# Kernel optimization log

Hardware: AMD Instinct MI355X
Metric: run time of the kernel (lower is better)

Reference implementation:

```python
import jax, jax.numpy as jnp
import numpy as np

D_MODEL = 1024
N_HEADS = 16
D_HEAD = D_MODEL // N_HEADS
D_FF = 4096
BATCH = 2
SEQ = 2048
EPS = 1e-5


def setup_inputs() -> dict:
    key = jax.random.key(0)
    ks = jax.random.split(key, 8)
    s = 0.02
    x = jax.random.normal(ks[0], (BATCH, SEQ, D_MODEL), dtype=jnp.float32)
    # Per-head projection weights, stacked: [H, d_head, d_model] (torch Linear stores (out,in))
    wq = jax.random.normal(ks[1], (N_HEADS, D_HEAD, D_MODEL), dtype=jnp.float32) * s
    wk = jax.random.normal(ks[2], (N_HEADS, D_HEAD, D_MODEL), dtype=jnp.float32) * s
    wv = jax.random.normal(ks[3], (N_HEADS, D_HEAD, D_MODEL), dtype=jnp.float32) * s
    wo = jax.random.normal(ks[4], (D_MODEL, D_MODEL), dtype=jnp.float32) * s
    w1 = jax.random.normal(ks[5], (D_FF, D_MODEL), dtype=jnp.float32) * s
    w2 = jax.random.normal(ks[6], (D_MODEL, D_FF), dtype=jnp.float32) * s
    ln1_g = jnp.ones((D_MODEL,), jnp.float32)
    ln1_b = jnp.zeros((D_MODEL,), jnp.float32)
    ln2_g = jnp.ones((D_MODEL,), jnp.float32)
    ln2_b = jnp.zeros((D_MODEL,), jnp.float32)
    return {"x": x, "wq": wq, "wk": wk, "wv": wv, "wo": wo,
            "w1": w1, "w2": w2, "ln1_g": ln1_g, "ln1_b": ln1_b,
            "ln2_g": ln2_g, "ln2_b": ln2_b}


def _layer_norm(x, g, b):
    mu = jnp.mean(x, axis=-1, keepdims=True)
    var = jnp.mean(jnp.square(x - mu), axis=-1, keepdims=True)
    return (x - mu) * jax.lax.rsqrt(var + EPS) * g + b


def _mha(h, wq, wk, wv, wo):
    # h: [b,s,d]; wq/wk/wv: [H,dh,d] -> q/k/v: [b,H,s,dh]
    q = jnp.einsum('bsd,hed->bhse', h, wq)
    k = jnp.einsum('bsd,hed->bhse', h, wk)
    v = jnp.einsum('bsd,hed->bhse', h, wv)
    scores = jnp.einsum('bhqe,bhke->bhqk', q, k) / jnp.sqrt(jnp.float32(D_HEAD))
    weights = jax.nn.softmax(scores, axis=-1)
    ctx = jnp.einsum('bhqk,bhke->bhqe', weights, v)  # [b,H,s,dh]
    # concat heads in order (head 0 first) -> [b,s,H*dh]
    concat = jnp.transpose(ctx, (0, 2, 1, 3)).reshape(h.shape[0], h.shape[1], D_MODEL)
    return concat @ wo.T


def reference(x, wq, wk, wv, wo, w1, w2, ln1_g, ln1_b, ln2_g, ln2_b):
    h = _layer_norm(x, ln1_g, ln1_b)
    attn_out = _mha(h, wq, wk, wv, wo)
    h2 = _layer_norm(x + attn_out, ln2_g, ln2_b)
    ff = jax.nn.gelu(h2 @ w1.T, approximate=False) @ w2.T
    return x + ff
```

## Files before the change

kernel.cpp:

```cpp
#include <hip/hip_runtime.h>
#include <hip/hip_bf16.h>
#include <math.h>

typedef __bf16 bf16_t;
typedef __bf16 bf16x8 __attribute__((ext_vector_type(8)));
typedef __bf16 bf16x4 __attribute__((ext_vector_type(4)));
typedef float f32x4 __attribute__((ext_vector_type(4)));
typedef unsigned int u32;
typedef u32 u32x2 __attribute__((ext_vector_type(2)));

#define DM 1024
#define SEQL 2048
#define NTOK 4096
#define QKVN 3072

__device__ __forceinline__ void gload_lds16(const bf16_t* g, bf16_t* l){
  __builtin_amdgcn_global_load_lds((const __attribute__((address_space(1))) void*)g,
                                   (__attribute__((address_space(3))) void*)l, 16, 0, 0);
}
__device__ __forceinline__ u32 ldsoff(const void* p){
  return (u32)(size_t)(__attribute__((address_space(3))) const void*)p;
}
__device__ __forceinline__ u32x2 tr64(u32 byte_off){
  u32x2 d;
  asm volatile("ds_read_b64_tr_b16 %0, %1" : "=v"(d) : "v"(byte_off));
  return d;
}
__device__ __forceinline__ u32 pack2(float a, float b){
  union{ __bf16 h[2]; u32 w; } z;
  z.h[0]=(__bf16)a; z.h[1]=(__bf16)b; return z.w;
}
__device__ __forceinline__ float gelu_fast(float x){
  const float y = 0.79788456f*(x + 0.044715f*x*x*x);
  float a = y*2.885390082f;
  a = fminf(fmaxf(a, -30.f), 30.f);
  const float t = __builtin_amdgcn_exp2f(a);
  const float th = (t-1.0f)*__builtin_amdgcn_rcpf(t+1.0f);
  return 0.5f*x*(1.0f+th);
}

__global__ __launch_bounds__(256) void prep_kernel(
    const float* __restrict__ wq, const float* __restrict__ wk,
    const float* __restrict__ wv, const float* __restrict__ wo,
    const float* __restrict__ w1, const float* __restrict__ w2,
    const float* __restrict__ x,  const float* __restrict__ g1,
    const float* __restrict__ b1,
    bf16_t* __restrict__ wqkv_b, bf16_t* __restrict__ wo_b,
    bf16_t* __restrict__ w1_b,   bf16_t* __restrict__ w2_b,
    bf16_t* __restrict__ h1)
{
  __shared__ float red[8];
  const int bid = blockIdx.x;
  const int t = threadIdx.x;
  if (bid < 12288){
    const int flat = (bid*256 + t)*4;
    const int seg = flat >> 20;
    const int off1m = flat & 1048575;
    const float* src; bf16_t* dst;
    if (seg < 3){
      src = (seg==0 ? wq : (seg==1 ? wk : wv)) + off1m;
      dst = wqkv_b + flat;
    } else if (seg == 3){
      src = wo + off1m;  dst = wo_b + off1m;
    } else if (seg < 8){
      src = w1 + (flat - 4*1048576);  dst = w1_b + (flat - 4*1048576);
    } else {
      src = w2 + (flat - 8*1048576);  dst = w2_b + (flat - 8*1048576);
    }
    const float4 v = *(const float4*)src;
    bf16x4 o; o[0]=(__bf16)v.x; o[1]=(__bf16)v.y; o[2]=(__bf16)v.z; o[3]=(__bf16)v.w;
    *(bf16x4*)dst = o;
  } else {
    const int row = bid - 12288;
    const float4 v = *(const float4*)(x + (size_t)row*DM + t*4);
    float s  = v.x+v.y+v.z+v.w;
    float sq = v.x*v.x+v.y*v.y+v.z*v.z+v.w*v.w;
    #pragma unroll
    for (int m=1;m<64;m<<=1){ s += __shfl_xor(s,m); sq += __shfl_xor(sq,m); }
    const int w = t>>6;
    if ((t&63)==0){ red[w]=s; red[4+w]=sq; }
    __syncthreads();
    s  = red[0]+red[1]+red[2]+red[3];
    sq = red[4]+red[5]+red[6]+red[7];
    const float mean = s*(1.f/DM);
    const float var  = sq*(1.f/DM) - mean*mean;
    const float rstd = rsqrtf(var + 1e-5f);
    const float4 gg = *(const float4*)(g1 + t*4);
    const float4 bb = *(const float4*)(b1 + t*4);
    bf16x4 o;
    o[0]=(__bf16)((v.x-mean)*rstd*gg.x+bb.x);
    o[1]=(__bf16)((v.y-mean)*rstd*gg.y+bb.y);
    o[2]=(__bf16)((v.z-mean)*rstd*gg.z+bb.z);
    o[3]=(__bf16)((v.w-mean)*rstd*gg.w+bb.w);
    *(bf16x4*)(h1 + (size_t)row*DM + t*4) = o;
  }
}

__global__ __launch_bounds__(256) void lnb_kernel(const bf16_t* __restrict__ in,
    const float* __restrict__ g, const float* __restrict__ bta,
    bf16_t* __restrict__ outp)
{
  const int row = blockIdx.x;
  const int t = threadIdx.x;
  const bf16x4 raw = *(const bf16x4*)(in + (size_t)row*DM + t*4);
  float4 v;
  v.x=(float)raw[0]; v.y=(float)raw[1]; v.z=(float)raw[2]; v.w=(float)raw[3];
  float s  = v.x+v.y+v.z+v.w;
  float sq = v.x*v.x+v.y*v.y+v.z*v.z+v.w*v.w;
  #pragma unroll
  for (int m=1;m<64;m<<=1){ s += __shfl_xor(s,m); sq += __shfl_xor(sq,m); }
  __shared__ float red[8];
  const int w = t>>6;
  if ((t&63)==0){ red[w]=s; red[4+w]=sq; }
  __syncthreads();
  s  = red[0]+red[1]+red[2]+red[3];
  sq = red[4]+red[5]+red[6]+red[7];
  const float mean = s*(1.f/DM);
  const float var  = sq*(1.f/DM) - mean*mean;
  const float rstd = rsqrtf(var + 1e-5f);
  const float4 gg = *(const float4*)(g + t*4);
  const float4 bb = *(const float4*)(bta + t*4);
  bf16x4 o;
  o[0]=(__bf16)((v.x-mean)*rstd*gg.x+bb.x);
  o[1]=(__bf16)((v.y-mean)*rstd*gg.y+bb.y);
  o[2]=(__bf16)((v.z-mean)*rstd*gg.z+bb.z);
  o[3]=(__bf16)((v.w-mean)*rstd*gg.w+bb.w);
  *(bf16x4*)(outp + (size_t)row*DM + t*4) = o;
}

__global__ __launch_bounds__(256) void red4_kernel(
    const bf16_t* __restrict__ p0, const bf16_t* __restrict__ p1,
    const bf16_t* __restrict__ p2, const bf16_t* __restrict__ p3,
    const float* __restrict__ x, float* __restrict__ outp)
{
  const int i = (blockIdx.x*256 + threadIdx.x)*8;
  const bf16x8 a0 = *(const bf16x8*)(p0 + i);
  const bf16x8 a1 = *(const bf16x8*)(p1 + i);
  const bf16x8 a2 = *(const bf16x8*)(p2 + i);
  const bf16x8 a3 = *(const bf16x8*)(p3 + i);
  #pragma unroll
  for (int h=0; h<2; h++){
    const float4 xs = *(const float4*)(x + i + h*4);
    float4 o;
    o.x = xs.x + ((float)a0[h*4+0]+(float)a1[h*4+0]) + ((float)a2[h*4+0]+(float)a3[h*4+0]);
    o.y = xs.y + ((float)a0[h*4+1]+(float)a1[h*4+1]) + ((float)a2[h*4+1]+(float)a3[h*4+1]);
    o.z = xs.z + ((float)a0[h*4+2]+(float)a1[h*4+2]) + ((float)a2[h*4+2]+(float)a3[h*4+2]);
    o.w = xs.w + ((float)a0[h*4+3]+(float)a1[h*4+3]) + ((float)a2[h*4+3]+(float)a3[h*4+3]);
    *(float4*)(outp + i + h*4) = o;
  }
}

template<int EPI>
__global__ __launch_bounds__(512, 2) void gemm8ph(
    const bf16_t* __restrict__ A, const bf16_t* __restrict__ Bw,
    void* __restrict__ c0, void* __restrict__ c1,
    void* __restrict__ c2, void* __restrict__ c3,
    int N, int K, int lda)
{
  __shared__ __align__(16) char ldsb[131072];
  const int tid = threadIdx.x, lane = tid&63, wid = tid>>6;
  const int q16 = lane&15, g = lane>>4;
  const int wm = wid>>2, wn = wid&3;

  const int flat = blockIdx.y*gridDim.x + blockIdx.x;
  const int xcd = flat&7, jj = flat>>3;
  const int NY = gridDim.y;
  const int jdiv = jj/NY, jmod = jj - jdiv*NY;
  const int bm = (xcd*2 + jdiv)*256, bn = jmod*256;
  const int sk = blockIdx.z;
  const int koff = sk*K;
  void* Cout = (sk==0) ? c0 : (sk==1) ? c1 : (sk==2) ? c2 : c3;

  int mloc, kloc;
  {
    const u32 L = tid*16;
    const u32 logical = L ^ (((L>>9)&1)<<5);
    mloc = (int)(logical>>6);
    kloc = (int)((logical&63)>>1);
  }
  const bf16_t* asrc = A  + (size_t)(bm + mloc)*lda + koff + kloc;
  const bf16_t* bsrc = Bw + (size_t)(bn + mloc)*lda + koff + kloc;
  const u32 laneOff = ((u32)(q16*64 + g*16)) ^ ((u32)(q16&8)<<2);

  f32x4 acc[8][4] = {};
  bf16x8 bv[4];

  auto stage = [&](int buf, int kh, int isB, int s){
    const bf16_t* src = isB ? bsrc : asrc;
    #pragma unroll
    for (int h2=0; h2<2; h2++)
      gload_lds16(src + (size_t)(h2*128)*lda + s*64 + kh*32,
                  (bf16_t*)(ldsb + buf*65536 + isB*32768 + kh*16384 + h2*8192 + tid*16));
  };

  stage(0,0,0,0); stage(0,0,1,0); stage(0,1,0,0); stage(0,1,1,0);
  stage(1,0,0,1); stage(1,0,1,1);
  asm volatile("s_waitcnt vmcnt(4)" ::: "memory");
  __builtin_amdgcn_s_barrier();

  const int NSTEP = K>>6;
  const int NIT = NSTEP>>1;

#define PHASE(BUF,KH,MH,DOST,SBUF,SKH,SISB,SSTEP,CK) { \
    bf16x8 av[4]; \
    const char* Ab_ = ldsb + (BUF)*65536 + (KH)*16384 + wm*8192; \
    _Pragma("unroll") for (int jx=0;jx<4;jx++) \
      av[jx] = *(const bf16x8*)(Ab_ + (((MH)*4+jx)<<10) + laneOff); \
    if ((MH)==0){ \
      const char* Bb_ = ldsb + (BUF)*65536 + 32768 + (KH)*16384 + (wn>>1)*8192; \
      _Pragma("unroll") for (int jx=0;jx<4;jx++) \
        bv[jx] = *(const bf16x8*)(Bb_ + ((((wn&1)*4)+jx)<<10) + laneOff); \
    } \
    if (DOST) stage(SBUF,SKH,SISB,SSTEP); \
    asm volatile("s_barrier" ::: "memory"); \
    asm volatile("s_waitcnt lgkmcnt(0)" ::: "memory"); \
    __builtin_amdgcn_s_setprio(1); \
    _Pragma("unroll") for (int jx=0;jx<4;jx++) \
      _Pragma("unroll") for (int j2=0;j2<4;j2++) \
        acc[(MH)*4+jx][j2] = __builtin_amdgcn_mfma_f32_16x16x32_bf16(av[jx], bv[j2], acc[(MH)*4+jx][j2],0,0,0); \
    __builtin_amdgcn_s_setprio(0); \
    if (CK){ if (nl) { asm volatile("s_waitcnt vmcnt(4)" ::: "memory"); } \
             else    { asm volatile("s_waitcnt vmcnt(0)" ::: "memory"); } } \
    asm volatile("s_barrier" ::: "memory"); }

  for (int it=0; it<NIT; it++){
    const int s0 = 2*it, s1 = s0+1;
    const bool nl = (it+1 < NIT);
    PHASE(0,0,0, 1,  1,1,0, s1,   0)
    PHASE(0,0,1, 1,  1,1,1, s1,   0)
    PHASE(0,1,0, nl, 0,0,0, s0+2, 0)
    PHASE(0,1,1, nl, 0,0,1, s0+2, 1)
    PHASE(1,0,0, nl, 0,1,0, s0+2, 0)
    PHASE(1,0,1, nl, 0,1,1, s0+2, 0)
    PHASE(1,1,0, nl, 1,0,0, s1+2, 0)
    PHASE(1,1,1, nl, 1,0,1, s1+2, 1)
  }
#undef PHASE

  #pragma unroll
  for (int fm=0; fm<8; fm++)
    #pragma unroll
    for (int fn=0; fn<4; fn++)
      #pragma unroll
      for (int i=0; i<4; i++){
        const int r = bm + wm*128 + fm*16 + g*4 + i;
        const int c = bn + wn*64 + fn*16 + q16;
        const size_t idx = (size_t)r*N + c;
        const float vv = acc[fm][fn][i];
        if constexpr (EPI==0){
          ((bf16_t*)Cout)[idx] = (__bf16)vv;
        } else {
          ((bf16_t*)Cout)[idx] = (__bf16)gelu_fast(vv);
        }
      }
}

template<int EPI>
__global__ __launch_bounds__(512, 2) void gemm128(
    const bf16_t* __restrict__ A, const bf16_t* __restrict__ Bw,
    void* __restrict__ Cout, const float* __restrict__ X,
    int N, int K)
{
  constexpr int BK = 32;
  __shared__ __align__(16) char ldsb[3*16384];
  const int tid = threadIdx.x, lane = tid&63, wid = tid>>6;
  const int q16 = lane&15, g = lane>>4;
  const int wm = wid>>2, wn = wid&3;

  const int flat = blockIdx.y*gridDim.x + blockIdx.x;
  const int xcd = flat&7, j = flat>>3;
  const int bm = ((xcd<<2) + (j>>3))*128, bn = (j&7)*128;

  int mloc, kloc;
  {
    const u32 L = tid*16;
    const u32 logical = L ^ (((L>>9)&1)<<5);
    mloc = (int)(logical>>6);
    kloc = (int)((logical&63)>>1);
  }
  const bf16_t* asrc = A  + (size_t)(bm + mloc)*K + kloc;
  const bf16_t* bsrc = Bw + (size_t)(bn + mloc)*K + kloc;
  const u32 laneOff = ((u32)(q16*64 + g*16)) ^ ((u32)(q16&8)<<2);

  f32x4 acc[4][2] = {};

  auto stageA = [&](int buf, int k0){
    gload_lds16(asrc + k0, (bf16_t*)(ldsb + buf*16384 + tid*16));
  };
  auto stageB = [&](int buf, int k0){
    gload_lds16(bsrc + k0, (bf16_t*)(ldsb + buf*16384 + 8192 + tid*16));
  };

  stageA(0,0); stageB(0,0);
  stageA(1,BK); stageB(1,BK);
  asm volatile("s_waitcnt vmcnt(2)" ::: "memory");
  __builtin_amdgcn_s_barrier();

  const int NT = K/BK;
  int bcur = 0;
  for (int kt=0; kt<NT; kt++){
    const int bstg = (bcur >= 1) ? bcur-1 : bcur+2;
    const char* Ab = ldsb + bcur*16384 + wm*4096;
    const char* Bb = ldsb + bcur*16384 + 8192 + wn*2048;
    const bool sOK = (kt+2 < NT);
    const int k0s = (kt+2)*BK;
    bf16x8 bv[2];
    #pragma unroll
    for (int p=0; p<2; p++){
      bf16x8 av[2];
      #pragma unroll
      for (int jx=0;jx<2;jx++)
        av[jx] = *(const bf16x8*)(Ab + ((p*2+jx)<<10) + laneOff);
      if (p==0){
        #pragma unroll
        for (int jx=0;jx<2;jx++)
          bv[jx] = *(const bf16x8*)(Bb + (jx<<10) + laneOff);
      }
      if (sOK){
        if (p==0) stageA(bstg,k0s);
        else      stageB(bstg,k0s);
      }
      asm volatile("s_barrier" ::: "memory");
      __builtin_amdgcn_s_setprio(1);
      #pragma unroll
      for (int jx=0;jx<2;jx++)
        #pragma unroll
        for (int j2=0;j2<2;j2++)
          acc[p*2+jx][j2] = __builtin_amdgcn_mfma_f32_16x16x32_bf16(av[jx], bv[j2], acc[p*2+jx][j2], 0,0,0);
      __builtin_amdgcn_s_setprio(0);
      if (p==1){
        if (sOK) asm volatile("s_waitcnt vmcnt(2)" ::: "memory");
        else     asm volatile("s_waitcnt vmcnt(0)" ::: "memory");
      }
      asm volatile("s_barrier" ::: "memory");
    }
    bcur = (bcur==2)?0:bcur+1;
  }

  #pragma unroll
  for (int fm=0; fm<4; fm++)
    #pragma unroll
    for (int fn=0; fn<2; fn++)
      #pragma unroll
      for (int i=0; i<4; i++){
        const int r = bm + wm*64 + fm*16 + g*4 + i;
        const int c = bn + wn*32 + fn*16 + q16;
        const size_t idx = (size_t)r*N + c;
        const float vv = X[idx] + acc[fm][fn][i];
        ((bf16_t*)Cout)[idx] = (__bf16)vv;
      }
}

__global__ __launch_bounds__(512, 4) void attn_kernel(
    const bf16_t* __restrict__ QKV, bf16_t* __restrict__ Ctx)
{
  __shared__ __align__(16) bf16_t Ks[2][128*64];
  __shared__ __align__(16) bf16_t Vs[2][32*4*72];
  const int tid = threadIdx.x, lane = tid&63, w = tid>>6;
  const int g = lane>>4, q16 = lane&15;
  const int bh = blockIdx.y, b = bh>>4, h = bh&15;
  const int qr0 = blockIdx.x*128 + w*16;
  const size_t tok0 = (size_t)b*SEQL;
  const int ch0 = h*64;

  bf16x8 aq[2];
  #pragma unroll
  for (int ks=0; ks<2; ks++){
    bf16x8 t = *(const bf16x8*)(QKV + (tok0+qr0+q16)*QKVN + ch0 + ks*32 + g*8);
    #pragma unroll
    for (int jx=0;jx<8;jx++) t[jx] = (__bf16)((float)t[jx]*0.18033688f);
    aq[ks] = t;
  }

  const int srow = tid>>3, sc8 = (tid&7)*8;
  const bf16_t* kptr_swz = QKV + (tok0+srow)*QKVN + 1024 + ch0 + (sc8 ^ ((srow&7)<<3));
  const bf16_t* vptr = QKV + (tok0+srow)*QKVN + 2048 + ch0 + sc8;
  const int vwoff = ((srow>>2)*4 + (sc8>>4))*72 + (srow&3)*16 + (sc8&15);

  float mrun = -1e30f, lrun = 0.f;
  f32x4 o[4] = {};

  #pragma unroll
  for (int it=0; it<2; it++)
    gload_lds16(kptr_swz + (size_t)(it*64)*QKVN, &Ks[0][tid*8 + it*4096]);
  bf16x8 vreg[2];
  #pragma unroll
  for (int it=0; it<2; it++)
    vreg[it] = *(const bf16x8*)(vptr + (size_t)(it*64)*QKVN);
  #pragma unroll
  for (int it=0; it<2; it++)
    *(bf16x8*)&Vs[0][vwoff + it*4608] = vreg[it];
  #pragma unroll
  for (int it=0; it<2; it++)
    vreg[it] = *(const bf16x8*)(vptr + (size_t)(128 + it*64)*QKVN);

  const int NT = SEQL/128;
  for (int t=0; t<NT; t++){
    __syncthreads();
    if (t+1 < NT){
      #pragma unroll
      for (int it=0; it<2; it++){
        gload_lds16(kptr_swz + (size_t)((t+1)*128 + it*64)*QKVN, &Ks[(t+1)&1][tid*8 + it*4096]);
        *(bf16x8*)&Vs[(t+1)&1][vwoff + it*4608] = vreg[it];
      }
      if (t+2 < NT){
        #pragma unroll
        for (int it=0; it<2; it++)
          vreg[it] = *(const bf16x8*)(vptr + (size_t)((t+2)*128 + it*64)*QKVN);
      }
    }
    const bf16_t* ksb = Ks[t&1];
    const u32 vs0 = ldsoff(&Vs[t&1][0]);

    f32x4 s[8] = {};
    __builtin_amdgcn_s_setprio(1);
    #pragma unroll
    for (int ks=0; ks<2; ks++){
      #pragma unroll
      for (int fn=0; fn<8; fn++){
        const int r = fn*16 + q16;
        const int ce = ks*32 + g*8;
        bf16x8 bk = *(const bf16x8*)&ksb[r*64 + (ce ^ ((r&7)<<3))];
        s[fn] = __builtin_amdgcn_mfma_f32_16x16x32_bf16(bk, aq[ks], s[fn], 0, 0, 0);
      }
    }
    __builtin_amdgcn_s_setprio(0);

    float mx = -1e30f;
    #pragma unroll
    for (int fn=0; fn<8; fn++){
      const float a = fmaxf(fmaxf(s[fn][0], s[fn][1]), s[fn][2]);
      mx = fmaxf(fmaxf(mx, a), s[fn][3]);
    }
    mx = fmaxf(mx, __shfl_xor(mx,16));
    mx = fmaxf(mx, __shfl_xor(mx,32));

    if (!__all(mx <= mrun + 11.54f)){
      const float mnew = fmaxf(mrun, mx);
      const float alpha = __builtin_amdgcn_exp2f(mrun - mnew);
      #pragma unroll
      for (int i=0;i<4;i++){
        const float ai = __shfl(alpha, g*4+i);
        o[0][i]*=ai; o[1][i]*=ai; o[2][i]*=ai; o[3][i]*=ai;
      }
      lrun *= alpha;
      mrun = mnew;
    }

    float rs = 0.f;
    u32 u[8][2];
    #pragma unroll
    for (int fn=0; fn<8; fn++){
      const float e0=__builtin_amdgcn_exp2f(s[fn][0]-mrun);
      const float e1=__builtin_amdgcn_exp2f(s[fn][1]-mrun);
      const float e2=__builtin_amdgcn_exp2f(s[fn][2]-mrun);
      const float e3=__builtin_amdgcn_exp2f(s[fn][3]-mrun);
      rs += (e0+e1)+(e2+e3);
      u[fn][0] = pack2(e0,e1);
      u[fn][1] = pack2(e2,e3);
    }
    rs += __shfl_xor(rs,16);
    rs += __shfl_xor(rs,32);
    lrun += rs;

    {
      u32x2 loA[4], hiA[4], loB[4], hiB[4];
      #pragma unroll
      for (int ne=0; ne<4; ne++){
        const u32 vb = vs0 + (u32)(((2*g*4 + ne)*72 + q16)*2);
        loA[ne] = tr64(vb);
        hiA[ne] = tr64(vb + 576);
      }
      #pragma unroll
      for (int ks=0; ks<4; ks++){
        union { u32 wd[4]; bf16x8 v; } pa;
        #pragma unroll
        for (int jj=0; jj<4; jj++){
          const int src = q16 + ((((g&1)<<1) + (jj>>1))<<4);
          const u32 a0 = (u32)__shfl((int)u[2*ks  ][jj&1], src);
          const u32 a1 = (u32)__shfl((int)u[2*ks+1][jj&1], src);
          pa.wd[jj] = (g&2) ? a1 : a0;
        }
        if (ks < 3){
          u32x2* nl_ = (ks&1) ? loA : loB;
          u32x2* nh_ = (ks&1) ? hiA : hiB;
          #pragma unroll
          for (int ne=0; ne<4; ne++){
            const u32 vb = vs0 + (u32)(((((ks+1)*8 + 2*g)*4 + ne)*72 + q16)*2);
            nl_[ne] = tr64(vb);
            nh_[ne] = tr64(vb + 576);
          }
          asm volatile("s_waitcnt lgkmcnt(8)" ::: "memory");
        } else {
          asm volatile("s_waitcnt lgkmcnt(0)" ::: "memory");
        }
        __builtin_amdgcn_sched_barrier(0);
        const u32x2* lo = (ks&1) ? loB : loA;
        const u32x2* hi = (ks&1) ? hiB : hiA;
        union { u32x2 u2[2]; bf16x8 v; } cc;
        __builtin_amdgcn_s_setprio(1);
        #pragma unroll
        for (int ne=0; ne<4; ne++){
          cc.u2[0]=lo[ne]; cc.u2[1]=hi[ne];
          o[ne] = __builtin_amdgcn_mfma_f32_16x16x32_bf16(pa.v, cc.v, o[ne], 0, 0, 0);
        }
        __builtin_amdgcn_s_setprio(0);
      }
    }
  }

  const float rl = 1.0f/lrun;
  #pragma unroll
  for (int i=0; i<4; i++){
    const float ri = __shfl(rl, g*4+i);
    #pragma unroll
    for (int ne=0; ne<4; ne++){
      const int r = qr0 + g*4 + i;
      Ctx[(tok0+r)*DM + ch0 + ne*16 + q16] = (__bf16)(o[ne][i]*ri);
    }
  }
}

extern "C" void kernel_launch(void* const* d_in, const int* in_sizes, int n_in,
                              void* d_out, int out_size, void* d_ws, size_t ws_size,
                              hipStream_t stream)
{
  (void)in_sizes; (void)n_in; (void)out_size; (void)ws_size;
  const float* x  = (const float*)d_in[0];
  const float* wq = (const float*)d_in[1];
  const float* wk = (const float*)d_in[2];
  const float* wv = (const float*)d_in[3];
  const float* wo = (const float*)d_in[4];
  const float* w1 = (const float*)d_in[5];
  const float* w2 = (const float*)d_in[6];
  const float* g1 = (const float*)d_in[7];
  const float* b1 = (const float*)d_in[8];
  const float* g2 = (const float*)d_in[9];
  const float* b2 = (const float*)d_in[10];
  float* out = (float*)d_out;
  char* ws = (char*)d_ws;
  const size_t MB = 1024ull*1024ull;

  bf16_t* wqkv_b = (bf16_t*)(ws);
  bf16_t* wo_b   = (bf16_t*)(ws + 6*MB);
  bf16_t* w1_b   = (bf16_t*)(ws + 8*MB);
  bf16_t* w2_b   = (bf16_t*)(ws + 16*MB);
  bf16_t* h1     = (bf16_t*)(ws + 24*MB);
  bf16_t* qkv    = (bf16_t*)(ws + 32*MB);
  bf16_t* ctx    = (bf16_t*)(ws + 56*MB);
  bf16_t* res2b  = (bf16_t*)(ws + 64*MB);
  bf16_t* h2     = h1;
  bf16_t* ffm    = (bf16_t*)(ws + 32*MB);
  bf16_t* p0     = (bf16_t*)(ws);
  bf16_t* p1     = (bf16_t*)(ws + 8*MB);
  bf16_t* p2     = (bf16_t*)(ws + 24*MB);
  bf16_t* p3     = (bf16_t*)(ws + 64*MB);

  prep_kernel<<<16384, 256, 0, stream>>>(wq, wk, wv, wo, w1, w2, x, g1, b1,
                                         wqkv_b, wo_b, w1_b, w2_b, h1);
  gemm8ph<0><<<dim3(16, 12), 512, 0, stream>>>(h1, wqkv_b, (void*)qkv, (void*)qkv,
                                               (void*)qkv, (void*)qkv, QKVN, 1024, 1024);
  attn_kernel<<<dim3(16, 32), 512, 0, stream>>>(qkv, ctx);
  gemm128<0><<<dim3(32, 8), 512, 0, stream>>>(ctx, wo_b, (void*)res2b, x, 1024, 1024);
  lnb_kernel<<<NTOK, 256, 0, stream>>>(res2b, g2, b2, h2);
  gemm8ph<2><<<dim3(16, 16), 512, 0, stream>>>(h2, w1_b, (void*)ffm, (void*)ffm,
                                               (void*)ffm, (void*)ffm, 4096, 1024, 1024);
  gemm8ph<0><<<dim3(16, 4, 4), 512, 0, stream>>>(ffm, w2_b, (void*)p0, (void*)p1,
                                                 (void*)p2, (void*)p3, 1024, 1024, 4096);
  red4_kernel<<<2048, 256, 0, stream>>>(p0, p1, p2, p3, x, out);
}
```

Before: 232.4 us.

## Split attention KV range in two with a separate log-sum-exp combine kernel

The attention kernel now splits each head's key/value sequence into two halves along a new grid z dimension, which doubles the block count. Each block uses 64-key tiles and half the shared memory, and the launch bound allows 8 blocks per CU instead of 4. Each split writes an unnormalized bf16 partial output plus its per-row max and sum. A new combine kernel merges the two partials with exp2 rescaling into the context buffer. This is meant to fix under-filled CUs in attention, at the cost of an extra launch, extra memory traffic for the partials, and rounding the unnormalized partials to bf16.

```diff
diff --git a/kernel.cpp b/kernel.cpp
--- a/kernel.cpp
+++ b/kernel.cpp
@@ -148,6 +148,29 @@
     o.w = xs.w + ((float)a0[h*4+3]+(float)a1[h*4+3]) + ((float)a2[h*4+3]+(float)a3[h*4+3]);
     *(float4*)(outp + i + h*4) = o;
   }
+}
+
+__global__ __launch_bounds__(256) void attn_comb(
+    const bf16_t* __restrict__ Op0, const bf16_t* __restrict__ Op1,
+    const float2* __restrict__ ml, bf16_t* __restrict__ Ctx)
+{
+  const int tok = blockIdx.x, t = threadIdx.x;
+  const int b = tok>>11, s = tok&2047;
+  const int h = t>>4;
+  const float2 m0 = ml[(b*16+h)*2048 + s];
+  const float2 m1 = ml[32*2048 + (b*16+h)*2048 + s];
+  const float M = fmaxf(m0.x, m1.x);
+  const float w0 = __builtin_amdgcn_exp2f(m0.x - M);
+  const float w1 = __builtin_amdgcn_exp2f(m1.x - M);
+  const float rl = 1.0f/(m0.y*w0 + m1.y*w1);
+  const size_t base = (size_t)tok*DM + t*4;
+  const bf16x4 o0 = *(const bf16x4*)(Op0 + base);
+  const bf16x4 o1 = *(const bf16x4*)(Op1 + base);
+  bf16x4 o;
+  #pragma unroll
+  for (int j=0;j<4;j++)
+    o[j] = (__bf16)((((float)o0[j])*w0 + ((float)o1[j])*w1)*rl);
+  *(bf16x4*)(Ctx + base) = o;
 }
 
 template<int EPI>
@@ -351,14 +374,16 @@
       }
 }
 
-__global__ __launch_bounds__(512, 4) void attn_kernel(
-    const bf16_t* __restrict__ QKV, bf16_t* __restrict__ Ctx)
-{
-  __shared__ __align__(16) bf16_t Ks[2][128*64];
-  __shared__ __align__(16) bf16_t Vs[2][32*4*72];
+__global__ __launch_bounds__(512, 8) void attn_kernel(
+    const bf16_t* __restrict__ QKV, bf16_t* __restrict__ Op0,
+    bf16_t* __restrict__ Op1, float2* __restrict__ ml)
+{
+  __shared__ __align__(16) bf16_t Ks[2][64*64];
+  __shared__ __align__(16) bf16_t Vs[2][16*4*72];
   const int tid = threadIdx.x, lane = tid&63, w = tid>>6;
   const int g = lane>>4, q16 = lane&15;
   const int bh = blockIdx.y, b = bh>>4, h = bh&15;
+  const int z = blockIdx.z;
   const int qr0 = blockIdx.x*128 + w*16;
   const size_t tok0 = (size_t)b*SEQL;
   const int ch0 = h*64;
@@ -373,51 +398,37 @@
   }
 
   const int srow = tid>>3, sc8 = (tid&7)*8;
-  const bf16_t* kptr_swz = QKV + (tok0+srow)*QKVN + 1024 + ch0 + (sc8 ^ ((srow&7)<<3));
-  const bf16_t* vptr = QKV + (tok0+srow)*QKVN + 2048 + ch0 + sc8;
+  const size_t zrow = tok0 + (size_t)(z<<10) + srow;
+  const bf16_t* kptr_swz = QKV + zrow*QKVN + 1024 + ch0 + (sc8 ^ ((srow&7)<<3));
+  const bf16_t* vptr = QKV + zrow*QKVN + 2048 + ch0 + sc8;
   const int vwoff = ((srow>>2)*4 + (sc8>>4))*72 + (srow&3)*16 + (sc8&15);
 
   float mrun = -1e30f, lrun = 0.f;
   f32x4 o[4] = {};
 
-  #pragma unroll
-  for (int it=0; it<2; it++)
-    gload_lds16(kptr_swz + (size_t)(it*64)*QKVN, &Ks[0][tid*8 + it*4096]);
-  bf16x8 vreg[2];
-  #pragma unroll
-  for (int it=0; it<2; it++)
-    vreg[it] = *(const bf16x8*)(vptr + (size_t)(it*64)*QKVN);
-  #pragma unroll
-  for (int it=0; it<2; it++)
-    *(bf16x8*)&Vs[0][vwoff + it*4608] = vreg[it];
-  #pragma unroll
-  for (int it=0; it<2; it++)
-    vreg[it] = *(const bf16x8*)(vptr + (size_t)(128 + it*64)*QKVN);
-
-  const int NT = SEQL/128;
+  gload_lds16(kptr_swz, &Ks[0][tid*8]);
+  bf16x8 vreg = *(const bf16x8*)vptr;
+  *(bf16x8*)&Vs[0][vwoff] = vreg;
+  vreg = *(const bf16x8*)(vptr + (size_t)64*QKVN);
+
+  const int NT = 1024/64;
   for (int t=0; t<NT; t++){
     __syncthreads();
     if (t+1 < NT){
-      #pragma unroll
-      for (int it=0; it<2; it++){
-        gload_lds16(kptr_swz + (size_t)((t+1)*128 + it*64)*QKVN, &Ks[(t+1)&1][tid*8 + it*4096]);
-        *(bf16x8*)&Vs[(t+1)&1][vwoff + it*4608] = vreg[it];
-      }
-      if (t+2 < NT){
-        #pragma unroll
-        for (int it=0; it<2; it++)
-          vreg[it] = *(const bf16x8*)(vptr + (size_t)((t+2)*128 + it*64)*QKVN);
-      }
+      gload_lds16(kptr_swz + (size_t)(t+1)*64*QKVN, &Ks[(t+1)&1][tid*8]);
+      *(bf16x8*)&Vs[(t+1)&1][vwoff] = vreg;
+      if (t+2 < NT)
+        vreg = *(const bf16x8*)(vptr + (size_t)(t+2)*64*QKVN);
     }
     const bf16_t* ksb = Ks[t&1];
     const u32 vs0 = ldsoff(&Vs[t&1][0]);
 
-    f32x4 s[8] = {};
+    f32x4 s[4] = {};
     __builtin_amdgcn_s_setprio(1);
     #pragma unroll
     for (int ks=0; ks<2; ks++){
       #pragma unroll
-      for (int fn=0; fn<8; fn++){
+      for (int fn=0; fn<4; fn++){
         const int r = fn*16 + q16;
         const int ce = ks*32 + g*8;
         bf16x8 bk = *(const bf16x8*)&ksb[r*64 + (ce ^ ((r&7)<<3))];
@@ -428,7 +439,7 @@
 
     float mx = -1e30f;
     #pragma unroll
-    for (int fn=0; fn<8; fn++){
+    for (int fn=0; fn<4; fn++){
       const float a = fmaxf(fmaxf(s[fn][0], s[fn][1]), s[fn][2]);
       mx = fmaxf(fmaxf(mx, a), s[fn][3]);
     }
@@ -448,9 +459,9 @@
     }
 
     float rs = 0.f;
-    u32 u[8][2];
-    #pragma unroll
-    for (int fn=0; fn<8; fn++){
+    u32 u[4][2];
+    #pragma unroll
+    for (int fn=0; fn<4; fn++){
       const float e0=__builtin_amdgcn_exp2f(s[fn][0]-mrun);
       const float e1=__builtin_amdgcn_exp2f(s[fn][1]-mrun);
       const float e2=__builtin_amdgcn_exp2f(s[fn][2]-mrun);
@@ -463,61 +474,48 @@
     rs += __shfl_xor(rs,32);
     lrun += rs;
 
-    {
-      u32x2 loA[4], hiA[4], loB[4], hiB[4];
+    #pragma unroll
+    for (int ks=0; ks<2; ks++){
+      u32x2 vlo[4], vhi[4];
       #pragma unroll
       for (int ne=0; ne<4; ne++){
-        const u32 vb = vs0 + (u32)(((2*g*4 + ne)*72 + q16)*2);
-        loA[ne] = tr64(vb);
-        hiA[ne] = tr64(vb + 576);
-      }
-      #pragma unroll
-      for (int ks=0; ks<4; ks++){
-        union { u32 wd[4]; bf16x8 v; } pa;
-        #pragma unroll
-        for (int jj=0; jj<4; jj++){
-          const int src = q16 + ((((g&1)<<1) + (jj>>1))<<4);
-          const u32 a0 = (u32)__shfl((int)u[2*ks  ][jj&1], src);
-          const u32 a1 = (u32)__shfl((int)u[2*ks+1][jj&1], src);
-          pa.wd[jj] = (g&2) ? a1 : a0;
-        }
-        if (ks < 3){
-          u32x2* nl_ = (ks&1) ? loA : loB;
-          u32x2* nh_ = (ks&1) ? hiA : hiB;
-          #pragma unroll
-          for (int ne=0; ne<4; ne++){
-            const u32 vb = vs0 + (u32)(((((ks+1)*8 + 2*g)*4 + ne)*72 + q16)*2);
-            nl_[ne] = tr64(vb);
-            nh_[ne] = tr64(vb + 576);
-          }
-          asm volatile("s_waitcnt lgkmcnt(8)" ::: "memory");
-        } else {
-          asm volatile("s_waitcnt lgkmcnt(0)" ::: "memory");
-        }
-        __builtin_amdgcn_sched_barrier(0);
-        const u32x2* lo = (ks&1) ? loB : loA;
-        const u32x2* hi = (ks&1) ? hiB : hiA;
-        union { u32x2 u2[2]; bf16x8 v; } cc;
-        __builtin_amdgcn_s_setprio(1);
-        #pragma unroll
-        for (int ne=0; ne<4; ne++){
-          cc.u2[0]=lo[ne]; cc.u2[1]=hi[ne];
-          o[ne] = __builtin_amdgcn_mfma_f32_16x16x32_bf16(pa.v, cc.v, o[ne], 0, 0, 0);
-        }
-        __builtin_amdgcn_s_setprio(0);
-      }
-    }
-  }
-
-  const float rl = 1.0f/lrun;
+        const u32 vb = vs0 + (u32)((((ks*8 + 2*g)*4 + ne)*72 + q16)*2);
+        vlo[ne] = tr64(vb);
+        vhi[ne] = tr64(vb + 576);
+      }
+      union { u32 wd[4]; bf16x8 v; } pa;
+      #pragma unroll
+      for (int jj=0; jj<4; jj++){
+        const int src = q16 + ((((g&1)<<1) + (jj>>1))<<4);
+        const u32 a0 = (u32)__shfl((int)u[2*ks  ][jj&1], src);
+        const u32 a1 = (u32)__shfl((int)u[2*ks+1][jj&1], src);
+        pa.wd[jj] = (g&2) ? a1 : a0;
+      }
+      asm volatile("s_waitcnt lgkmcnt(0)" ::: "memory");
+      __builtin_amdgcn_sched_barrier(0);
+      union { u32x2 u2[2]; bf16x8 v; } cc;
+      __builtin_amdgcn_s_setprio(1);
+      #pragma unroll
+      for (int ne=0; ne<4; ne++){
+        cc.u2[0]=vlo[ne]; cc.u2[1]=vhi[ne];
+        o[ne] = __builtin_amdgcn_mfma_f32_16x16x32_bf16(pa.v, cc.v, o[ne], 0, 0, 0);
+      }
+      __builtin_amdgcn_s_setprio(0);
+    }
+  }
+
+  bf16_t* Op = z ? Op1 : Op0;
   #pragma unroll
   for (int i=0; i<4; i++){
-    const float ri = __shfl(rl, g*4+i);
     #pragma unroll
     for (int ne=0; ne<4; ne++){
       const int r = qr0 + g*4 + i;
-      Ctx[(tok0+r)*DM + ch0 + ne*16 + q16] = (__bf16)(o[ne][i]*ri);
-    }
+      Op[(tok0+r)*DM + ch0 + ne*16 + q16] = (__bf16)o[ne][i];
+    }
+  }
+  if (lane < 16){
+    float2 v; v.x = mrun; v.y = lrun;
+    ml[(z*32 + bh)*2048 + qr0 + q16] = v;
   }
 }
 
@@ -551,6 +549,9 @@
   bf16_t* res2b  = (bf16_t*)(ws + 64*MB);
   bf16_t* h2     = h1;
   bf16_t* ffm    = (bf16_t*)(ws + 32*MB);
+  bf16_t* op0    = (bf16_t*)(ws + 24*MB);
+  bf16_t* op1    = (bf16_t*)(ws + 64*MB);
+  float2* mlb    = (float2*)(ws);
   bf16_t* p0     = (bf16_t*)(ws);
   bf16_t* p1     = (bf16_t*)(ws + 8*MB);
   bf16_t* p2     = (bf16_t*)(ws + 24*MB);
@@ -560,7 +561,8 @@
                                          wqkv_b, wo_b, w1_b, w2_b, h1);
   gemm8ph<0><<<dim3(16, 12), 512, 0, stream>>>(h1, wqkv_b, (void*)qkv, (void*)qkv,
                                                (void*)qkv, (void*)qkv, QKVN, 1024, 1024);
-  attn_kernel<<<dim3(16, 32), 512, 0, stream>>>(qkv, ctx);
+  attn_kernel<<<dim3(16, 32, 2), 512, 0, stream>>>(qkv, op0, op1, mlb);
+  attn_comb<<<NTOK, 256, 0, stream>>>(op0, op1, mlb, ctx);
   gemm128<0><<<dim3(32, 8), 512, 0, stream>>>(ctx, wo_b, (void*)res2b, x, 1024, 1024);
   lnb_kernel<<<NTOK, 256, 0, stream>>>(res2b, g2, b2, h2);
   gemm8ph<2><<<dim3(16, 16), 512, 0, stream>>>(h2, w1_b, (void*)ffm, (void*)ffm,
```

After: 264.8 us. 13.9% more time.
